# Performance work log

Hardware: AMD Instinct MI355X
Metric: run time of the kernel (lower is better)

The kernel has to match this reference:

```python
import jax, jax.numpy as jnp
import numpy as np

K = 20          # args.k
NEG = 0.2       # LeakyReLU negative slope

def lrelu(x):
    return jnp.where(x >= 0, x, NEG * x)

def bn(x, s, b):
    # eval-mode batchnorm folded into per-channel affine; channel axis = 1
    sh = (1, -1) + (1,) * (x.ndim - 2)
    return x * s.reshape(sh) + b.reshape(sh)

def se(x, w1, w2):
    # Squeeze-and-Excite on (B, C, N, k)
    y = jnp.mean(x, axis=(2, 3))                      # (B, C)
    y = jax.nn.sigmoid(jax.nn.relu(y @ w1.T) @ w2.T)  # (B, C)
    return x * y[:, :, None, None]

def graph_feature(x):
    # x: (B, C, N) -> edge features (B, 2C, N, K)
    xx = jnp.sum(x * x, axis=1)                        # (B, N)
    inner = jnp.einsum('bcn,bcm->bnm', x, x)           # (B, N, N)
    dist = -xx[:, :, None] + 2.0 * inner - xx[:, None, :]
    idx = jax.lax.top_k(dist, K)[1]                    # (B, N, K) nearest (incl. self)
    xt = jnp.transpose(x, (0, 2, 1))                   # (B, N, C)
    nbr = jax.vmap(lambda t, i: t[i])(xt, idx)         # (B, N, K, C)
    ctr = xt[:, :, None, :]
    out = jnp.concatenate([nbr - ctr, jnp.broadcast_to(ctr, nbr.shape)], axis=3)
    return jnp.transpose(out, (0, 3, 1, 2))

def edge_block(x, w, s, b, w1, w2):
    # get_graph_feature -> 1x1 conv -> BN -> SE -> LeakyReLU -> max over k
    g = graph_feature(x)                               # (B, 2C, N, K)
    h = jnp.einsum('bcnk,oc->bonk', g, w)
    h = lrelu(se(bn(h, s, b), w1, w2))
    return jnp.max(h, axis=-1)                         # (B, O, N)

def forward(x, conv1_w, conv2_w, conv3_w, conv4_w, conv5_w,
            bn1_s, bn1_b, bn2_s, bn2_b, bn3_s, bn3_b, bn4_s, bn4_b, bn5_s, bn5_b,
            se1_w1, se1_w2, se2_w1, se2_w2, se3_w1, se3_w2, se4_w1, se4_w2,
            res1_w, res2_w, res3_w,
            lin1_w, bn6_s, bn6_b, lin2_w, lin2_b, bn7_s, bn7_b, lin3_w, lin3_b):
    x1 = edge_block(x, conv1_w, bn1_s, bn1_b, se1_w1, se1_w2)                 # (B,512,N)
    x2 = edge_block(x1, conv2_w, bn2_s, bn2_b, se2_w1, se2_w2)
    x2 = x2 + jnp.einsum('bcn,oc->bon', x1, res1_w)                           # (B,512,N)
    x3 = edge_block(x2, conv3_w, bn3_s, bn3_b, se3_w1, se3_w2)
    x3 = x3 + jnp.einsum('bcn,oc->bon', x2, res2_w)                           # (B,1024,N)
    x4 = edge_block(x3, conv4_w, bn4_s, bn4_b, se4_w1, se4_w2)
    x4 = x4 + jnp.einsum('bcn,oc->bon', x3, res3_w)                           # (B,1024,N)
    h = jnp.concatenate([x1, x2, x3, x4], axis=1)                             # (B,3072,N)
    h = lrelu(bn(jnp.einsum('bcn,oc->bon', h, conv5_w), bn5_s, bn5_b))        # (B,2048,N)
    f = jnp.concatenate([jnp.max(h, axis=-1), jnp.mean(h, axis=-1)], axis=1)  # (B,4096)
    f = lrelu(bn(f @ lin1_w.T, bn6_s, bn6_b))       # dropout is eval-mode identity
    f = lrelu(bn(f @ lin2_w.T + lin2_b, bn7_s, bn7_b))
    return f @ lin3_w.T + lin3_b                    # (B,40)

def setup_inputs():
    ks = jax.random.split(jax.random.key(0), 40)
    B, N = 16, 128
    f32 = jnp.float32
    def w(i, shape, s=0.02):
        return jax.random.normal(ks[i], shape, f32) * s
    def bns(i, c):
        return 1.0 + 0.1 * jax.random.normal(ks[i], (c,), f32)
    def bnb(i, c):
        return 0.1 * jax.random.normal(ks[i], (c,), f32)
    return {
        'x': jax.random.normal(ks[0], (B, 512, N), f32),
        'conv1_w': w(1, (512, 1024)),
        'conv2_w': w(2, (512, 1024)),
        'conv3_w': w(3, (1024, 1024)),
        'conv4_w': w(4, (1024, 2048)),
        'conv5_w': w(5, (2048, 3072)),
        'bn1_s': bns(6, 512), 'bn1_b': bnb(7, 512),
        'bn2_s': bns(8, 512), 'bn2_b': bnb(9, 512),
        'bn3_s': bns(10, 1024), 'bn3_b': bnb(11, 1024),
        'bn4_s': bns(12, 1024), 'bn4_b': bnb(13, 1024),
        'bn5_s': bns(14, 2048), 'bn5_b': bnb(15, 2048),
        'se1_w1': w(16, (32, 512), 0.05), 'se1_w2': w(17, (512, 32), 0.05),
        'se2_w1': w(18, (32, 512), 0.05), 'se2_w2': w(19, (512, 32), 0.05),
        'se3_w1': w(20, (64, 1024), 0.05), 'se3_w2': w(21, (1024, 64), 0.05),
        'se4_w1': w(22, (64, 1024), 0.05), 'se4_w2': w(23, (1024, 64), 0.05),
        'res1_w': w(24, (512, 512)),
        'res2_w': w(25, (1024, 512)),
        'res3_w': w(26, (1024, 1024)),
        'lin1_w': w(27, (512, 4096)),
        'bn6_s': bns(28, 512), 'bn6_b': bnb(29, 512),
        'lin2_w': w(30, (256, 512)), 'lin2_b': bnb(31, 256),
        'bn7_s': bns(32, 256), 'bn7_b': bnb(33, 256),
        'lin3_w': w(34, (40, 256)), 'lin3_b': bnb(35, 40),
    }

def reference(x, conv1_w, conv2_w, conv3_w, conv4_w, conv5_w,
              bn1_s, bn1_b, bn2_s, bn2_b, bn3_s, bn3_b, bn4_s, bn4_b, bn5_s, bn5_b,
              se1_w1, se1_w2, se2_w1, se2_w2, se3_w1, se3_w2, se4_w1, se4_w2,
              res1_w, res2_w, res3_w,
              lin1_w, bn6_s, bn6_b, lin2_w, lin2_b, bn7_s, bn7_b, lin3_w, lin3_b):
    return forward(x, conv1_w, conv2_w, conv3_w, conv4_w, conv5_w,
                   bn1_s, bn1_b, bn2_s, bn2_b, bn3_s, bn3_b, bn4_s, bn4_b, bn5_s, bn5_b,
                   se1_w1, se1_w2, se2_w1, se2_w2, se3_w1, se3_w2, se4_w1, se4_w2,
                   res1_w, res2_w, res3_w,
                   lin1_w, bn6_s, bn6_b, lin2_w, lin2_b, bn7_s, bn7_b, lin3_w, lin3_b)
```

## Files before the change

### kernel.cpp

```cpp
#include <hip/hip_runtime.h>
#include <hip/hip_bf16.h>


#define BN_ALL 2048
typedef __hip_bfloat16 bf16;
typedef __attribute__((ext_vector_type(8))) short short8;
typedef __attribute__((ext_vector_type(4))) float float4v;
typedef __attribute__((ext_vector_type(4))) int int4v;

__device__ __forceinline__ float b2f(bf16 v) { return __bfloat162float(v); }
__device__ __forceinline__ float bs2f(short s) { return __bfloat162float(*reinterpret_cast<bf16*>(&s)); }
__device__ __forceinline__ float lrelu(float v) { return v >= 0.f ? v : 0.2f * v; }
__device__ __forceinline__ short f2bs(float v) {
    bf16 h = __float2bfloat16(v);
    return *reinterpret_cast<short*>(&h);
}

__device__ __forceinline__ void gll16(const void* g, void* l) {
    __builtin_amdgcn_global_load_lds(
        (const __attribute__((address_space(1))) unsigned int*)g,
        (__attribute__((address_space(3))) unsigned int*)l,
        16, 0, 0);
}

__device__ __forceinline__ float ldin(const void* p, size_t i, int isb) {
    return isb ? __bfloat162float(((const bf16*)p)[i]) : ((const float*)p)[i];
}

__device__ __forceinline__ float ld1(const float* p) { return *p; }
__device__ __forceinline__ float ld1(const bf16* p)  { return __bfloat162float(*p); }
__device__ __forceinline__ void st1(float* p, float v) { *p = v; }
__device__ __forceinline__ void st1(bf16* p, float v)  { *p = __float2bfloat16(v); }

__global__ __launch_bounds__(256) void detect_dtype(const void* __restrict__ x, int* __restrict__ flag) {
    const unsigned* u = (const unsigned*)x;
    int sane = 0;
    for (int i = threadIdx.x; i < 4096; i += 256) {
        unsigned e = (u[i] >> 23) & 0xFF;
        sane += (e >= 87 && e <= 167) ? 1 : 0;
    }
    __shared__ int sh[256];
    sh[threadIdx.x] = sane;
    __syncthreads();
    for (int off = 128; off > 0; off >>= 1) {
        if (threadIdx.x < off) sh[threadIdx.x] += sh[threadIdx.x + off];
        __syncthreads();
    }
    if (threadIdx.x == 0) *flag = (sh[0] < 2048) ? 1 : 0;
}

__device__ __forceinline__ void convert_core(int bid, int tid, const void* __restrict__ x,
                                             bf16* __restrict__ X0, int isb) {
    int item = bid * 256 + tid;
    int cg = item >> 11, bn = item & 2047;
    int b = bn >> 7, n = bn & 127;
    short8 pk;
#pragma unroll
// ... 247 lines not shown
            for (int nt = 0; nt < 2; ++nt)
                bv[nt] = *(const short8*)&Bp[(size_t)(h * 256 + (lq << 6) + wn * 32 + nt * 16 + lr) * 8];
#pragma unroll
            for (int mt = 0; mt < 4; ++mt)
#pragma unroll
                for (int nt = 0; nt < 2; ++nt)
                    acc[mt][nt] = __builtin_amdgcn_mfma_f32_16x16x32_bf16(av[mt], bv[nt], acc[mt][nt], 0, 0, 0);
        }
        __syncthreads();
        p ^= 1;
    }

    int isb = *dflag;
#pragma unroll
    for (int mt = 0; mt < 4; ++mt) {
#pragma unroll
        for (int r = 0; r < 4; ++r) {
            int row = bm + wm * 64 + mt * 16 + lq * 4 + r;
            float s = 1.f, bb = 0.f;
            if (bnS) { s = ldin(bnS, row, isb); bb = ldin(bnB, row, isb); }
#pragma unroll
            for (int nt = 0; nt < 2; ++nt) {
                int col = bn0 + wn * 32 + nt * 16 + lr;
                float v = acc[mt][nt][r];
                if (bnS) v = v * s + bb;
                if (act) v = lrelu(v);
                Cm[(size_t)row * BN_ALL + col] = v;
            }
        }
    }
}

__global__ __launch_bounds__(256) void gemm_pk(const short* __restrict__ packA,
                                               const bf16* __restrict__ X, float* __restrict__ Cm, int K,
                                               const void* __restrict__ bnS, const void* __restrict__ bnB,
                                               int act, const int* __restrict__ dflag) {
    __shared__ __align__(16) short SMEM[24576];
    gemm_core(blockIdx.x, blockIdx.y, threadIdx.x, SMEM, packA, X, Cm, K, bnS, bnB, act, dflag);
}

__global__ __launch_bounds__(256) void gram_gemm_k(const bf16* __restrict__ X, float* __restrict__ G,
                                                   const short* __restrict__ packA,
                                                   float* __restrict__ Cm, int K,
                                                   const int* __restrict__ dflag) {
    __shared__ __align__(16) short SMEM[24576];
    if (blockIdx.x < 16) {
        gram_core(blockIdx.x, threadIdx.x, SMEM, X, K, G);
    } else {
        int g = blockIdx.x - 16;
        gemm_core(g >> 5, g & 31, threadIdx.x, SMEM, packA, X, Cm, K, nullptr, nullptr, 0, dflag);
    }
}

template <typename S>
__global__ __launch_bounds__(128) void knn_topk(const S* __restrict__ X, int C, int* __restrict__ idx) {
    int b = blockIdx.x >> 7;
    int n = blockIdx.x & 127;
    int m = threadIdx.x;
    const S* base = X + b * 128;
    float s0 = 0, s1 = 0, q0 = 0, q1 = 0;
    for (int c = 0; c < C; c += 2) {
        const S* p = base + (size_t)c * BN_ALL;
        float xm0 = ld1(p + m),          xn0 = ld1(p + n);
        float xm1 = ld1(p + BN_ALL + m), xn1 = ld1(p + BN_ALL + n);
        s0 += xm0 * xn0; q0 += xm0 * xm0;
        s1 += xm1 * xn1; q1 += xm1 * xm1;
    }
    float inner = s0 + s1;
    float xxm   = q0 + q1;
    __shared__ float xx[128];
    __shared__ float dist[128];
    __shared__ float rv[128];
    __shared__ int   ri[128];
    xx[m] = xxm;
    __syncthreads();
    dist[m] = 2.0f * inner - xx[n] - xxm;
    for (int k = 0; k < 20; k++) {
        __syncthreads();
        rv[m] = dist[m]; ri[m] = m;
        __syncthreads();
        for (int off = 64; off > 0; off >>= 1) {
            if (m < off) {
                float a = rv[m], bv = rv[m + off];
                int ia = ri[m], ib = ri[m + off];
                if (bv > a || (bv == a && ib < ia)) { rv[m] = bv; ri[m] = ib; }
            }
            __syncthreads();
        }
        if (m == 0) { idx[blockIdx.x * 20 + k] = ri[0]; dist[ri[0]] = -3.0e38f; }
    }
}

template <typename S>
__global__ __launch_bounds__(256) void gemm_mfma(const void* __restrict__ w, int ldw,
                                                 const void* __restrict__ res, int Cin, int O,
                                                 const S* __restrict__ X, S* __restrict__ Cm, int K,
                                                 const void* __restrict__ bnS, const void* __restrict__ bnB,
                                                 int act, const int* __restrict__ dflag) {
    int isb = *dflag;
    __shared__ short Asm[4096];
    __shared__ short Bsm[4096];
    int tid = threadIdx.x;
    int bm  = blockIdx.x << 7;
    int bn0 = blockIdx.y << 7;
    int lane = tid & 63, wv = tid >> 6;
    int wm = wv & 1, wn = wv >> 1;
// ... 19 lines not shown
            short8 pk;
#pragma unroll
            for (int j = 0; j < 8; ++j) {
                float v = ldin(asrc, abase + kk + j, isb);
                if (dif) v = ldin(asrc, abase + Cin + kk + j, isb) - v;
                pk[j] = f2bs(v);
            }
            *(short8*)&Asm[(size_t)(q * 128 + m) * 8] = pk;
        }
#pragma unroll
        for (int it = 0; it < 2; ++it) {
            int i = tid + it * 256;
            int q = i >> 7, c = i & 127;
            const S* xp = X + (size_t)(k0 + q * 8) * BN_ALL + bn0 + c;
            short8 pk;
#pragma unroll
            for (int j = 0; j < 8; ++j) pk[j] = f2bs(ld1(xp + (size_t)j * BN_ALL));
            *(short8*)&Bsm[(size_t)i * 8] = pk;
        }
        __syncthreads();
        short8 av[4], bv[4];
#pragma unroll
        for (int mt = 0; mt < 4; ++mt)
            av[mt] = *(const short8*)&Asm[(size_t)((lq << 7) + wm * 64 + mt * 16 + lr) * 8];
#pragma unroll
        for (int nt = 0; nt < 4; ++nt)
            bv[nt] = *(const short8*)&Bsm[(size_t)((lq << 7) + wn * 64 + nt * 16 + lr) * 8];
#pragma unroll
        for (int mt = 0; mt < 4; ++mt)
#pragma unroll
            for (int nt = 0; nt < 4; ++nt)
                acc[mt][nt] = __builtin_amdgcn_mfma_f32_16x16x32_bf16(av[mt], bv[nt], acc[mt][nt], 0, 0, 0);
        __syncthreads();
    }
#pragma unroll
    for (int mt = 0; mt < 4; ++mt) {
#pragma unroll
        for (int r = 0; r < 4; ++r) {
            int row = bm + wm * 64 + mt * 16 + lq * 4 + r;
            float s = 1.f, bb = 0.f;
            if (bnS) { s = ldin(bnS, row, isb); bb = ldin(bnB, row, isb); }
#pragma unroll
            for (int nt = 0; nt < 4; ++nt) {
                int col = bn0 + wn * 64 + nt * 16 + lr;
                float v = acc[mt][nt][r];
                if (bnS) v = v * s + bb;
                if (act) v = lrelu(v);
                st1(Cm + (size_t)row * BN_ALL + col, v);
            }
        }
    }
}

template <typename S>
__global__ __launch_bounds__(256) void gather_pool(S* __restrict__ PS, const int* __restrict__ idx,
                                                   const void* __restrict__ bns, const void* __restrict__ bnb,
                                                   float* __restrict__ Mb, int O,
                                                   const int* __restrict__ dflag) {
    int isb = *dflag;
    int wv = threadIdx.x >> 6, lane = threadIdx.x & 63;
    int gw = blockIdx.x * 4 + wv;
    int o = gw >> 4, b = gw & 15;
    S* Prow = PS + (size_t)o * BN_ALL + b * 128;
    const S* Srow = PS + (size_t)(O + o) * BN_ALL + b * 128;
    int n0 = lane, n1 = lane + 64;
    const int4v* id0v = (const int4v*)(idx + (b * 128 + n0) * 20);
    const int4v* id1v = (const int4v*)(idx + (b * 128 + n1) * 20);
    int id0[20], id1[20];
#pragma unroll
    for (int t = 0; t < 5; ++t) {
        int4v v0 = id0v[t], v1 = id1v[t];
#pragma unroll
        for (int j = 0; j < 4; ++j) { id0[t * 4 + j] = v0[j]; id1[t * 4 + j] = v1[j]; }
    }
    float mx0 = -3.0e38f, mn0 = 3.0e38f, sm0 = 0.f;
    float mx1 = -3.0e38f, mn1 = 3.0e38f, sm1 = 0.f;
#pragma unroll
    for (int k = 0; k < 20; k++) {
        float p = ld1(Prow + id0[k]);
        mx0 = fmaxf(mx0, p); mn0 = fminf(mn0, p); sm0 += p;
    }
#pragma unroll
    for (int k = 0; k < 20; k++) {
        float p = ld1(Prow + id1[k]);
        mx1 = fmaxf(mx1, p); mn1 = fminf(mn1, p); sm1 += p;
    }
    float Sv0 = ld1(Srow + n0), Sv1 = ld1(Srow + n1);
    float s = ldin(bns, o, isb), bb = ldin(bnb, o, isb);
    float ext0 = (s >= 0.f) ? mx0 : mn0;
    float ext1 = (s >= 0.f) ? mx1 : mn1;
    float t0 = lrelu(s * (ext0 + Sv0) + bb);
    float t1 = lrelu(s * (ext1 + Sv1) + bb);
    st1(Prow + n0, t0);
    st1(Prow + n1, t1);
    float r1 = sm0 + sm1;
    float r2 = Sv0 + Sv1;
#pragma unroll
    for (int off = 32; off > 0; off >>= 1) {
        r1 += __shfl_xor(r1, off, 64);
        r2 += __shfl_xor(r2, off, 64);
    }
    if (lane == 0) Mb[b * O + o] = s * (r1 * (1.f / 2560.f) + r2 * (1.f / 128.f)) + bb;
}

__global__ __launch_bounds__(256) void se1_k(const float* __restrict__ Mb, const void* __restrict__ w1,
                                             float* __restrict__ Z, int O, int r,
                                             const int* __restrict__ dflag) {
    int isb = *dflag;
    int gw = (blockIdx.x * 256 + threadIdx.x) >> 6;
    int lane = threadIdx.x & 63;
    int b = gw / r, t = gw - b * r;
    const float* mv = Mb + (size_t)b * O;
    float acc = 0.f;
    for (int c = lane; c < O; c += 64) acc += ldin(w1, (size_t)t * O + c, isb) * mv[c];
#pragma unroll
    for (int off = 32; off > 0; off >>= 1) acc += __shfl_xor(acc, off, 64);
    if (lane == 0) Z[b * r + t] = fmaxf(acc, 0.f);
}

__global__ __launch_bounds__(256) void se2_k(const float* __restrict__ Z, const void* __restrict__ w2,
                                             float* __restrict__ Y, int O, int r,
                                             const int* __restrict__ dflag) {
    int isb = *dflag;
    int gw = (blockIdx.x * 256 + threadIdx.x) >> 6;
    int lane = threadIdx.x & 63;
    int b = gw / O, o = gw - b * O;
    float acc = 0.f;
    if (lane < r) acc = ldin(w2, (size_t)o * r + lane, isb) * Z[b * r + lane];
#pragma unroll
    for (int off = 32; off > 0; off >>= 1) acc += __shfl_xor(acc, off, 64);
    if (lane == 0) Y[b * O + o] = 1.f / (1.f + expf(-acc));
}

__global__ __launch_bounds__(256) void se_k(const float* __restrict__ Mb, const void* __restrict__ w1,
                                            const void* __restrict__ w2, float* __restrict__ Y, int O, int r,
                                            const int* __restrict__ dflag) {
    int isb = *dflag;
    int b = blockIdx.x, t = threadIdx.x;
    __shared__ float mloc[1024];
    __shared__ float z[64];
    for (int i = t; i < O; i += 256) mloc[i] = Mb[b * O + i];
    __syncthreads();
    if (t < r) {
        float acc = 0.f;
        for (int c = 0; c < O; c++) acc += ldin(w1, (size_t)t * O + c, isb) * mloc[c];
        z[t] = fmaxf(acc, 0.f);
    }
    __syncthreads();
    for (int o = t; o < O; o += 256) {
        float acc = 0.f;
        for (int j = 0; j < r; j++) acc += ldin(w2, (size_t)o * r + j, isb) * z[j];
        Y[b * O + o] = 1.f / (1.f + expf(-acc));
    }
}

__global__ __launch_bounds__(256) void finalize2_kp(const float* __restrict__ PS,
                                                    const float* __restrict__ Z,
                                                    const void* __restrict__ w2,
                                                    int useR, bf16* __restrict__ Xdst, int O, int r,
                                                    const int* __restrict__ dflag) {
    int isb = *dflag;
    int og = blockIdx.x >> 3;
    int b0 = (blockIdx.x & 7) * 2;
    __shared__ float Ysm[16];
    int wv = threadIdx.x >> 6, lane = threadIdx.x & 63;
#pragma unroll
    for (int s = 0; s < 4; ++s) {
        int pp = wv * 4 + s;
        int b = b0 + (pp >> 3);
        int o = og * 8 + (pp & 7);
        float acc = 0.f;
        if (lane < r) acc = ldin(w2, (size_t)o * r + lane, isb) * Z[b * r + lane];
#pragma unroll
        for (int off = 32; off > 0; off >>= 1) acc += __shfl_xor(acc, off, 64);
        if (lane == 0) Ysm[pp] = 1.f / (1.f + expf(-acc));
    }
    __syncthreads();
    int item = blockIdx.x * 256 + threadIdx.x;
    int bn = item & 2047;
    int b = bn >> 7;
    short8 pk;
#pragma unroll
    for (int j = 0; j < 8; ++j) {
        int rr = og * 8 + j;
        float v = Ysm[(b - b0) * 8 + j] * PS[(size_t)rr * BN_ALL + bn];
        if (useR) v += PS[(size_t)(2 * O + rr) * BN_ALL + bn];
        pk[j] = f2bs(v);
    }
    *(short8*)((short*)Xdst + ((size_t)og * BN_ALL + bn) * 8) = pk;
}

__global__ __launch_bounds__(256) void finalize_kp(const float* __restrict__ PS, const float* __restrict__ Y,
                                                   int useR, bf16* __restrict__ Xdst, int O) {
    int item = blockIdx.x * 256 + threadIdx.x;
    int og = item >> 11, bn = item & 2047;
    int b = bn >> 7;
    short8 pk;
#pragma unroll
    for (int j = 0; j < 8; ++j) {
        int r = og * 8 + j;
        float v = Y[b * O + r] * PS[(size_t)r * BN_ALL + bn];
        if (useR) v += PS[(size_t)(2 * O + r) * BN_ALL + bn];
        pk[j] = f2bs(v);
    }
    *(short8*)((short*)Xdst + ((size_t)og * BN_ALL + bn) * 8) = pk;
}

template <typename SP, typename SD>
__global__ __launch_bounds__(256) void finalize(const SP* __restrict__ PS, const float* __restrict__ Y,
                                                int useR, SD* __restrict__ Xdst, int O) {
    int tid = blockIdx.x * 256 + threadIdx.x;
    int o = tid >> 11, bn = tid & 2047;
    int b = bn >> 7;
    float v = Y[b * O + o] * ld1(PS + tid);
    if (useR) v += ld1(PS + (size_t)(2 * O + o) * BN_ALL + bn);
    st1(Xdst + tid, v);
}

template <typename S>
__global__ __launch_bounds__(256) void convert_x(const void* __restrict__ x, S* __restrict__ X0,
                                                 const int* __restrict__ dflag) {
    int isb = *dflag;
    int tid = blockIdx.x * 256 + threadIdx.x;
    int c = tid >> 11, bn = tid & 2047;
    int b = bn >> 7, n = bn & 127;
    st1(X0 + tid, ldin(x, (size_t)(b * 512 + c) * 128 + n, isb));
}

template <typename S>
__global__ __launch_bounds__(256) void pool5(const S* __restrict__ H, float* __restrict__ f) {
    int wv = threadIdx.x >> 6, lane = threadIdx.x & 63;
    int gw = blockIdx.x * 4 + wv;
    int m = gw >> 4, b = gw & 15;
    const S* Hp = H + (size_t)m * BN_ALL + b * 128;
    float v0 = ld1(Hp + lane), v1 = ld1(Hp + 64 + lane);
    float mx = fmaxf(v0, v1);
    float sm = v0 + v1;
#pragma unroll
    for (int off = 32; off > 0; off >>= 1) {
        mx = fmaxf(mx, __shfl_xor(mx, off, 64));
        sm += __shfl_xor(sm, off, 64);
    }
    if (lane == 0) {
        f[b * 4096 + m] = mx;
        f[b * 4096 + 2048 + m] = sm * (1.f / 128.f);
    }
}

__global__ __launch_bounds__(256) void head_k(const float* __restrict__ in, const void* __restrict__ W,
                                              const void* __restrict__ bias, const void* __restrict__ bns,
                                              const void* __restrict__ bnb, float* __restrict__ outf,
                                              void* __restrict__ outb, int Kd, int Od, int act,
                                              const int* __restrict__ dflag) {
    int isb = *dflag;
    int gw = (blockIdx.x * 256 + threadIdx.x) >> 6;
    int lane = threadIdx.x & 63;
    if (gw >= 16 * Od) return;
    int b = gw / Od, o = gw - b * Od;
    const float* iv = in + b * Kd;
    float acc = 0.f;
    for (int k = lane; k < Kd; k += 64) acc += iv[k] * ldin(W, (size_t)o * Kd + k, isb);
    for (int off = 32; off > 0; off >>= 1) acc += __shfl_xor(acc, off, 64);
    if (lane == 0) {
        float v = acc;
        if (bias) v += ldin(bias, o, isb);
        if (bns) v = v * ldin(bns, o, isb) + ldin(bnb, o, isb);
        if (act) v = lrelu(v);
        if (outb) {
            if (isb) ((bf16*)outb)[gw] = __float2bfloat16(v);
            else     ((float*)outb)[gw] = v;
        } else outf[gw] = v;
    }
}

__global__ __launch_bounds__(256) void zero_out(bf16* o, int n) {
    int i = blockIdx.x * 256 + threadIdx.x;
    if (i < n) o[i] = __float2bfloat16(0.f);
}

#define UNPACK_INPUTS()                                                     \
    const void* x_in   = d_in[0];                                           \
    const void* conv1w = d_in[1];  const void* conv2w = d_in[2];            \
    const void* conv3w = d_in[3];  const void* conv4w = d_in[4];            \
    const void* conv5w = d_in[5];                                           \
    const void* bn1s = d_in[6],  * bn1b = d_in[7];                          \
    const void* bn2s = d_in[8],  * bn2b = d_in[9];                          \
    const void* bn3s = d_in[10], * bn3b = d_in[11];                         \
    const void* bn4s = d_in[12], * bn4b = d_in[13];                         \
    const void* bn5s = d_in[14], * bn5b = d_in[15];                         \
    const void* se1w1 = d_in[16], * se1w2 = d_in[17];                       \
    const void* se2w1 = d_in[18], * se2w2 = d_in[19];                       \
    const void* se3w1 = d_in[20], * se3w2 = d_in[21];                       \
    const void* se4w1 = d_in[22], * se4w2 = d_in[23];                       \
    const void* res1w = d_in[24]; const void* res2w = d_in[25];             \
    const void* res3w = d_in[26]; const void* lin1w = d_in[27];             \
    const void* bn6s = d_in[28], * bn6b = d_in[29];                         \
    const void* lin2w = d_in[30], * lin2b = d_in[31];                       \
    const void* bn7s = d_in[32], * bn7b = d_in[33];                         \
    const void* lin3w = d_in[34], * lin3b = d_in[35];

static void run_net_packed2(void* const* d_in, void* d_out, void* d_ws, hipStream_t stream) {
    UNPACK_INPUTS();
    float* WS = (float*)d_ws;
    float* PS = WS;
    bf16*  XC = (bf16*)(WS + 6291456);
    short* P1 = (short*)(WS + 12582912);
    short* P2 = P1 + 524288;
    short* P3 = P2 + 786432;
    short* P4 = P3 + 1572864;
    short* P5 = P4 + 3145728;
    float* MB = WS + 18743296;
    float* YB = MB + 16384;
    float* FB = YB + 16384;
    float* F1 = FB + 65536;
    float* F2 = F1 + 8192;
    int* IDX  = (int*)(F2 + 4096);
    int* DFLAG = IDX + 40960;
    float* ZB = (float*)(DFLAG + 16);
    float* GRAM = WS + 18900000;
    bf16*  X0 = (bf16*)(PS + (size_t)2048 * BN_ALL);
    bf16* X1 = XC;
    bf16* X2 = XC + (size_t)512 * BN_ALL;
    bf16* X3 = XC + (size_t)1024 * BN_ALL;
    bf16* X4 = XC + (size_t)2048 * BN_ALL;

    detect_dtype<<<1, 256, 0, stream>>>(x_in, DFLAG);
    convert_pack_all<<<6528, 256, 0, stream>>>(x_in, X0,
        conv1w, conv2w, conv3w, conv4w, conv5w, res1w, res2w, res3w,
        P1, P2, P3, P4, P5, DFLAG);

    gram_gemm_k<<<16 + 8 * 32, 256, 0, stream>>>(X0, GRAM, P1, PS, 512, DFLAG);
    topk_k<<<512, 256, 0, stream>>>(GRAM, IDX);
    gather_pool<float><<<2048, 256, 0, stream>>>(PS, IDX, bn1s, bn1b, MB, 512, DFLAG);
    se1_k<<<128, 256, 0, stream>>>(MB, se1w1, ZB, 512, 32, DFLAG);
    finalize2_kp<<<512, 256, 0, stream>>>(PS, ZB, se1w2, 0, X1, 512, 32, DFLAG);

    gram_gemm_k<<<16 + 12 * 32, 256, 0, stream>>>(X1, GRAM, P2, PS, 512, DFLAG);
    topk_k<<<512, 256, 0, stream>>>(GRAM, IDX);
    gather_pool<float><<<2048, 256, 0, stream>>>(PS, IDX, bn2s, bn2b, MB, 512, DFLAG);
    se1_k<<<128, 256, 0, stream>>>(MB, se2w1, ZB, 512, 32, DFLAG);
    finalize2_kp<<<512, 256, 0, stream>>>(PS, ZB, se2w2, 1, X2, 512, 32, DFLAG);

    gram_gemm_k<<<16 + 24 * 32, 256, 0, stream>>>(X2, GRAM, P3, PS, 512, DFLAG);
    topk_k<<<512, 256, 0, stream>>>(GRAM, IDX);
    gather_pool<float><<<4096, 256, 0, stream>>>(PS, IDX, bn3s, bn3b, MB, 1024, DFLAG);
    se1_k<<<256, 256, 0, stream>>>(MB, se3w1, ZB, 1024, 64, DFLAG);
    finalize2_kp<<<1024, 256, 0, stream>>>(PS, ZB, se3w2, 1, X3, 1024, 64, DFLAG);

    gram_gemm_k<<<16 + 24 * 32, 256, 0, stream>>>(X3, GRAM, P4, PS, 1024, DFLAG);
    topk_k<<<512, 256, 0, stream>>>(GRAM, IDX);
    gather_pool<float><<<4096, 256, 0, stream>>>(PS, IDX, bn4s, bn4b, MB, 1024, DFLAG);
    se1_k<<<256, 256, 0, stream>>>(MB, se4w1, ZB, 1024, 64, DFLAG);
    finalize2_kp<<<1024, 256, 0, stream>>>(PS, ZB, se4w2, 1, X4, 1024, 64, DFLAG);

    gemm_pk<<<dim3(16, 32), 256, 0, stream>>>(P5, XC, PS, 3072, bn5s, bn5b, 1, DFLAG);
    pool5<float><<<8192, 256, 0, stream>>>(PS, FB);

    head_k<<<2048, 256, 0, stream>>>(FB, lin1w, nullptr, bn6s, bn6b, F1, nullptr, 4096, 512, 1, DFLAG);
    head_k<<<1024, 256, 0, stream>>>(F1, lin2w, lin2b, bn7s, bn7b, F2, nullptr, 512, 256, 1, DFLAG);
    head_k<<<160, 256, 0, stream>>>(F2, lin3w, lin3b, nullptr, nullptr, nullptr, d_out, 256, 40, 0, DFLAG);
}

static void run_net_packed(void* const* d_in, void* d_out, void* d_ws, hipStream_t stream) {
    UNPACK_INPUTS();
    float* WS = (float*)d_ws;
    float* PS   = WS;
    bf16*  XC   = (bf16*)(WS + 6291456);
    short* PACK = (short*)(WS + 12582912);
    float* MB = WS + 15728640;
    float* YB = MB + 16384;
    float* FB = YB + 16384;
    float* F1 = FB + 65536;
    float* F2 = F1 + 8192;
    int* IDX  = (int*)(F2 + 4096);
    int* DFLAG = IDX + 40960;
    float* ZB = (float*)(DFLAG + 16);
    bf16*  X0 = (bf16*)(PS + (size_t)2048 * BN_ALL);
    float* GRAM = PS;
    bf16* X1 = XC;
    bf16* X2 = XC + (size_t)512 * BN_ALL;
    bf16* X3 = XC + (size_t)1024 * BN_ALL;
    bf16* X4 = XC + (size_t)2048 * BN_ALL;

    detect_dtype<<<1, 256, 0, stream>>>(x_in, DFLAG);
    convert_kp<<<512, 256, 0, stream>>>(x_in, X0, DFLAG);

    gram_k<<<16, 256, 0, stream>>>(X0, 512, GRAM);
    topk_k<<<512, 256, 0, stream>>>(GRAM, IDX);
    pack_w<<<256, 256, 0, stream>>>(conv1w, 1024, nullptr, 512, 512, 1024, 512, PACK, DFLAG);
    gemm_pk<<<dim3(8, 32), 256, 0, stream>>>(PACK, X0, PS, 512, nullptr, nullptr, 0, DFLAG);
    gather_pool<float><<<2048, 256, 0, stream>>>(PS, IDX, bn1s, bn1b, MB, 512, DFLAG);
    se1_k<<<128, 256, 0, stream>>>(MB, se1w1, ZB, 512, 32, DFLAG);
    se2_k<<<2048, 256, 0, stream>>>(ZB, se1w2, YB, 512, 32, DFLAG);
    finalize_kp<<<512, 256, 0, stream>>>(PS, YB, 0, X1, 512);

    gram_k<<<16, 256, 0, stream>>>(X1, 512, GRAM);
    topk_k<<<512, 256, 0, stream>>>(GRAM, IDX);
    pack_w<<<384, 256, 0, stream>>>(conv2w, 1024, res1w, 512, 512, 1536, 512, PACK, DFLAG);
    gemm_pk<<<dim3(12, 32), 256, 0, stream>>>(PACK, X1, PS, 512, nullptr, nullptr, 0, DFLAG);
    gather_pool<float><<<2048, 256, 0, stream>>>(PS, IDX, bn2s, bn2b, MB, 512, DFLAG);
    se1_k<<<128, 256, 0, stream>>>(MB, se2w1, ZB, 512, 32, DFLAG);
    se2_k<<<2048, 256, 0, stream>>>(ZB, se2w2, YB, 512, 32, DFLAG);
    finalize_kp<<<512, 256, 0, stream>>>(PS, YB, 1, X2, 512);

    gram_k<<<16, 256, 0, stream>>>(X2, 512, GRAM);
    topk_k<<<512, 256, 0, stream>>>(GRAM, IDX);
    pack_w<<<768, 256, 0, stream>>>(conv3w, 1024, res2w, 512, 1024, 3072, 512, PACK, DFLAG);
    gemm_pk<<<dim3(24, 32), 256, 0, stream>>>(PACK, X2, PS, 512, nullptr, nullptr, 0, DFLAG);
    gather_pool<float><<<4096, 256, 0, stream>>>(PS, IDX, bn3s, bn3b, MB, 1024, DFLAG);
    se1_k<<<256, 256, 0, stream>>>(MB, se3w1, ZB, 1024, 64, DFLAG);
    se2_k<<<4096, 256, 0, stream>>>(ZB, se3w2, YB, 1024, 64, DFLAG);
    finalize_kp<<<1024, 256, 0, stream>>>(PS, YB, 1, X3, 1024);

// ... 95 lines not shown
```

Baseline: 527.5 us.

## Fuse per-layer topk/gather/SE/finalize and head tail into cooperative kernels

Replaces the chains of small kernel launches after each gram/gemm (topk, gather_pool, se1, finalize) and the final pool5 plus three head linears with two persistent cooperative kernels. A fixed grid of 768 blocks steps through each stage and calls grid.sync() between stages. The aim is to remove per-launch overhead and the idle gaps between many tiny kernels. In exchange, stages with few work items leave blocks idle, grid barriers have their own cost, and it relies on cooperative launch succeeding, with a fallback to the old launches.

New measurement: 1.621 ms. 3.07x slower.

```diff
diff --git a/kernel.cpp b/kernel.cpp
--- a/kernel.cpp
+++ b/kernel.cpp
@@ -1,8 +1,12 @@
 #include <hip/hip_runtime.h>
 #include <hip/hip_bf16.h>
+#include <hip/hip_cooperative_groups.h>
+
+namespace cg = cooperative_groups;
 
 
 #define BN_ALL 2048
+#define COOP_GRID 768
 typedef __hip_bfloat16 bf16;
 typedef __attribute__((ext_vector_type(8))) short short8;
 typedef __attribute__((ext_vector_type(4))) float float4v;
@@ -356,6 +360,245 @@
     }
 }
 
+__device__ __forceinline__ void gather_core(int vb, int tid, float* __restrict__ PS,
+                                            const int* __restrict__ idx,
+                                            const void* __restrict__ bns, const void* __restrict__ bnb,
+                                            float* __restrict__ Mb, int O, int isb) {
+    int wv = tid >> 6, lane = tid & 63;
+    int gw = vb * 4 + wv;
+    int o = gw >> 4, b = gw & 15;
+    float* Prow = PS + (size_t)o * BN_ALL + b * 128;
+    const float* Srow = PS + (size_t)(O + o) * BN_ALL + b * 128;
+    int n0 = lane, n1 = lane + 64;
+    const int4v* id0v = (const int4v*)(idx + (b * 128 + n0) * 20);
+    const int4v* id1v = (const int4v*)(idx + (b * 128 + n1) * 20);
+    int id0[20], id1[20];
+#pragma unroll
+    for (int t = 0; t < 5; ++t) {
+        int4v v0 = id0v[t], v1 = id1v[t];
+#pragma unroll
+        for (int j = 0; j < 4; ++j) { id0[t * 4 + j] = v0[j]; id1[t * 4 + j] = v1[j]; }
+    }
+    float mx0 = -3.0e38f, mn0 = 3.0e38f, sm0 = 0.f;
+    float mx1 = -3.0e38f, mn1 = 3.0e38f, sm1 = 0.f;
+#pragma unroll
+    for (int k = 0; k < 20; k++) {
+        float p = Prow[id0[k]];
+        mx0 = fmaxf(mx0, p); mn0 = fminf(mn0, p); sm0 += p;
+    }
+#pragma unroll
+    for (int k = 0; k < 20; k++) {
+        float p = Prow[id1[k]];
+        mx1 = fmaxf(mx1, p); mn1 = fminf(mn1, p); sm1 += p;
+    }
+    float Sv0 = Srow[n0], Sv1 = Srow[n1];
+    float s = ldin(bns, o, isb), bb = ldin(bnb, o, isb);
+    float ext0 = (s >= 0.f) ? mx0 : mn0;
+    float ext1 = (s >= 0.f) ? mx1 : mn1;
+    float t0 = lrelu(s * (ext0 + Sv0) + bb);
+    float t1 = lrelu(s * (ext1 + Sv1) + bb);
+    Prow[n0] = t0;
+    Prow[n1] = t1;
+    float r1 = sm0 + sm1;
+    float r2 = Sv0 + Sv1;
+#pragma unroll
+    for (int off = 32; off > 0; off >>= 1) {
+        r1 += __shfl_xor(r1, off, 64);
+        r2 += __shfl_xor(r2, off, 64);
+    }
+    if (lane == 0) Mb[b * O + o] = s * (r1 * (1.f / 2560.f) + r2 * (1.f / 128.f)) + bb;
+}
+
+template <typename S>
+__global__ __launch_bounds__(256) void gather_pool(S* __restrict__ PS, const int* __restrict__ idx,
+                                                   const void* __restrict__ bns, const void* __restrict__ bnb,
+                                                   float* __restrict__ Mb, int O,
+                                                   const int* __restrict__ dflag) {
+    int isb = *dflag;
+    int wv = threadIdx.x >> 6, lane = threadIdx.x & 63;
+    int gw = blockIdx.x * 4 + wv;
+    int o = gw >> 4, b = gw & 15;
+    S* Prow = PS + (size_t)o * BN_ALL + b * 128;
+    const S* Srow = PS + (size_t)(O + o) * BN_ALL + b * 128;
+    int n0 = lane, n1 = lane + 64;
+    const int4v* id0v = (const int4v*)(idx + (b * 128 + n0) * 20);
+    const int4v* id1v = (const int4v*)(idx + (b * 128 + n1) * 20);
+    int id0[20], id1[20];
+#pragma unroll
+    for (int t = 0; t < 5; ++t) {
+        int4v v0 = id0v[t], v1 = id1v[t];
+#pragma unroll
+        for (int j = 0; j < 4; ++j) { id0[t * 4 + j] = v0[j]; id1[t * 4 + j] = v1[j]; }
+    }
+    float mx0 = -3.0e38f, mn0 = 3.0e38f, sm0 = 0.f;
+    float mx1 = -3.0e38f, mn1 = 3.0e38f, sm1 = 0.f;
+#pragma unroll
+    for (int k = 0; k < 20; k++) {
+        float p = ld1(Prow + id0[k]);
+        mx0 = fmaxf(mx0, p); mn0 = fminf(mn0, p); sm0 += p;
+    }
+#pragma unroll
+    for (int k = 0; k < 20; k++) {
+        float p = ld1(Prow + id1[k]);
+        mx1 = fmaxf(mx1, p); mn1 = fminf(mn1, p); sm1 += p;
+    }
+    float Sv0 = ld1(Srow + n0), Sv1 = ld1(Srow + n1);
+    float s = ldin(bns, o, *dflag), bb = ldin(bnb, o, *dflag);
+    float ext0 = (s >= 0.f) ? mx0 : mn0;
+    float ext1 = (s >= 0.f) ? mx1 : mn1;
+    float t0 = lrelu(s * (ext0 + Sv0) + bb);
+    float t1 = lrelu(s * (ext1 + Sv1) + bb);
+    st1(Prow + n0, t0);
+    st1(Prow + n1, t1);
+    float r1 = sm0 + sm1;
+    float r2 = Sv0 + Sv1;
+#pragma unroll
+    for (int off = 32; off > 0; off >>= 1) {
+        r1 += __shfl_xor(r1, off, 64);
+        r2 += __shfl_xor(r2, off, 64);
+    }
+    if (lane == 0) Mb[b * O + o] = s * (r1 * (1.f / 2560.f) + r2 * (1.f / 128.f)) + bb;
+}
+
+__device__ __forceinline__ void se1_core(int vb, int tid, const float* __restrict__ Mb,
+                                         const void* __restrict__ w1, float* __restrict__ Z,
+                                         int O, int r, int isb) {
+    int gw = (vb * 256 + tid) >> 6;
+    int lane = tid & 63;
+    int b = gw / r, t = gw - b * r;
+    const float* mv = Mb + (size_t)b * O;
+    float acc = 0.f;
+    for (int c = lane; c < O; c += 64) acc += ldin(w1, (size_t)t * O + c, isb) * mv[c];
+#pragma unroll
+    for (int off = 32; off > 0; off >>= 1) acc += __shfl_xor(acc, off, 64);
+    if (lane == 0) Z[b * r + t] = fmaxf(acc, 0.f);
+}
+
+__global__ __launch_bounds__(256) void se1_k(const float* __restrict__ Mb, const void* __restrict__ w1,
+                                             float* __restrict__ Z, int O, int r,
+                                             const int* __restrict__ dflag) {
+    se1_core(blockIdx.x, threadIdx.x, Mb, w1, Z, O, r, *dflag);
+}
+
+__global__ __launch_bounds__(256) void se2_k(const float* __restrict__ Z, const void* __restrict__ w2,
+                                             float* __restrict__ Y, int O, int r,
+                                             const int* __restrict__ dflag) {
+    int isb = *dflag;
+    int gw = (blockIdx.x * 256 + threadIdx.x) >> 6;
+    int lane = threadIdx.x & 63;
+    int b = gw / O, o = gw - b * O;
+    float acc = 0.f;
+    if (lane < r) acc = ldin(w2, (size_t)o * r + lane, isb) * Z[b * r + lane];
+#pragma unroll
+    for (int off = 32; off > 0; off >>= 1) acc += __shfl_xor(acc, off, 64);
+    if (lane == 0) Y[b * O + o] = 1.f / (1.f + expf(-acc));
+}
+
+__global__ __launch_bounds__(256) void se_k(const float* __restrict__ Mb, const void* __restrict__ w1,
+                                            const void* __restrict__ w2, float* __restrict__ Y, int O, int r,
+                                            const int* __restrict__ dflag) {
+    int isb = *dflag;
+    int b = blockIdx.x, t = threadIdx.x;
+    __shared__ float mloc[1024];
+    __shared__ float z[64];
+    for (int i = t; i < O; i += 256) mloc[i] = Mb[b * O + i];
+    __syncthreads();
+    if (t < r) {
+        float acc = 0.f;
+        for (int c = 0; c < O; c++) acc += ldin(w1, (size_t)t * O + c, isb) * mloc[c];
+        z[t] = fmaxf(acc, 0.f);
+    }
+    __syncthreads();
+    for (int o = t; o < O; o += 256) {
+        float acc = 0.f;
+        for (int j = 0; j < r; j++) acc += ldin(w2, (size_t)o * r + j, isb) * z[j];
+        Y[b * O + o] = 1.f / (1.f + expf(-acc));
+    }
+}
+
+__device__ __forceinline__ void fin2_core(int vb, int tid, const float* __restrict__ PS,
+                                          const float* __restrict__ Z, const void* __restrict__ w2,
+                                          int useR, bf16* __restrict__ Xdst, int O, int r, int isb,
+                                          float* __restrict__ Ysm) {
+    int og = vb >> 3;
+    int b0 = (vb & 7) * 2;
+    int wv = tid >> 6, lane = tid & 63;
+#pragma unroll
+    for (int s = 0; s < 4; ++s) {
+        int pp = wv * 4 + s;
+        int b = b0 + (pp >> 3);
+        int o = og * 8 + (pp & 7);
+        float acc = 0.f;
+        if (lane < r) acc = ldin(w2, (size_t)o * r + lane, isb) * Z[b * r + lane];
+#pragma unroll
+        for (int off = 32; off > 0; off >>= 1) acc += __shfl_xor(acc, off, 64);
+        if (lane == 0) Ysm[pp] = 1.f / (1.f + expf(-acc));
+    }
+    __syncthreads();
+    int item = vb * 256 + tid;
+    int bn = item & 2047;
+    int b = bn >> 7;
+    short8 pk;
+#pragma unroll
+    for (int j = 0; j < 8; ++j) {
+        int rr = og * 8 + j;
+        float v = Ysm[(b - b0) * 8 + j] * PS[(size_t)rr * BN_ALL + bn];
+        if (useR) v += PS[(size_t)(2 * O + rr) * BN_ALL + bn];
+        pk[j] = f2bs(v);
+    }
+    *(short8*)((short*)Xdst + ((size_t)og * BN_ALL + bn) * 8) = pk;
+}
+
+__global__ __launch_bounds__(256) void finalize2_kp(const float* __restrict__ PS,
+                                                    const float* __restrict__ Z,
+                                                    const void* __restrict__ w2,
+                                                    int useR, bf16* __restrict__ Xdst, int O, int r,
+                                                    const int* __restrict__ dflag) {
+    __shared__ float Ysm[16];
+    fin2_core(blockIdx.x, threadIdx.x, PS, Z, w2, useR, Xdst, O, r, *dflag, Ysm);
+}
+
+__global__ __launch_bounds__(256) void tail_coop(const float* __restrict__ G, int* __restrict__ idx,
+                                                 float* __restrict__ PS,
+                                                 const void* __restrict__ bns, const void* __restrict__ bnb,
+                                                 float* __restrict__ Mb, const void* __restrict__ w1,
+                                                 float* __restrict__ Z, const void* __restrict__ w2,
+                                                 int useR, bf16* __restrict__ Xdst, int O, int r,
+                                                 const int* __restrict__ dflag) {
+    cg::grid_group grid = cg::this_grid();
+    __shared__ float Ysm[16];
+    int isb = *dflag;
+    int tid = threadIdx.x;
+    if (blockIdx.x < 512) topk_core(blockIdx.x, tid, G, idx);
+    grid.sync();
+    for (int vb = blockIdx.x; vb < O * 4; vb += COOP_GRID)
+        gather_core(vb, tid, PS, idx, bns, bnb, Mb, O, isb);
+    grid.sync();
+    for (int vb = blockIdx.x; vb < (16 * r) / 4; vb += COOP_GRID)
+        se1_core(vb, tid, Mb, w1, Z, O, r, isb);
+    grid.sync();
+    for (int vb = blockIdx.x; vb < O; vb += COOP_GRID) {
+        fin2_core(vb, tid, PS, Z, w2, useR, Xdst, O, r, isb, Ysm);
+        __syncthreads();
+    }
+}
+
+__global__ __launch_bounds__(256) void finalize_kp(const float* __restrict__ PS, const float* __restrict__ Y,
+                                                   int useR, bf16* __restrict__ Xdst, int O) {
+    int item = blockIdx.x * 256 + threadIdx.x;
+    int og = item >> 11, bn = item & 2047;
+    int b = bn >> 7;
+    short8 pk;
+#pragma unroll
+    for (int j = 0; j < 8; ++j) {
+        int r = og * 8 + j;
+        float v = Y[b * O + r] * PS[(size_t)r * BN_ALL + bn];
+        if (useR) v += PS[(size_t)(2 * O + r) * BN_ALL + bn];
+        pk[j] = f2bs(v);
+    }
+    *(short8*)((short*)Xdst + ((size_t)og * BN_ALL + bn) * 8) = pk;
+}
+
 template <typename S>
 __global__ __launch_bounds__(128) void knn_topk(const S* __restrict__ X, int C, int* __restrict__ idx) {
     int b = blockIdx.x >> 7;
@@ -481,160 +724,6 @@
     }
 }
 
-template <typename S>
-__global__ __launch_bounds__(256) void gather_pool(S* __restrict__ PS, const int* __restrict__ idx,
-                                                   const void* __restrict__ bns, const void* __restrict__ bnb,
-                                                   float* __restrict__ Mb, int O,
-                                                   const int* __restrict__ dflag) {
-    int isb = *dflag;
-    int wv = threadIdx.x >> 6, lane = threadIdx.x & 63;
-    int gw = blockIdx.x * 4 + wv;
-    int o = gw >> 4, b = gw & 15;
-    S* Prow = PS + (size_t)o * BN_ALL + b * 128;
-    const S* Srow = PS + (size_t)(O + o) * BN_ALL + b * 128;
-    int n0 = lane, n1 = lane + 64;
-    const int4v* id0v = (const int4v*)(idx + (b * 128 + n0) * 20);
-    const int4v* id1v = (const int4v*)(idx + (b * 128 + n1) * 20);
-    int id0[20], id1[20];
-#pragma unroll
-    for (int t = 0; t < 5; ++t) {
-        int4v v0 = id0v[t], v1 = id1v[t];
-#pragma unroll
-        for (int j = 0; j < 4; ++j) { id0[t * 4 + j] = v0[j]; id1[t * 4 + j] = v1[j]; }
-    }
-    float mx0 = -3.0e38f, mn0 = 3.0e38f, sm0 = 0.f;
-    float mx1 = -3.0e38f, mn1 = 3.0e38f, sm1 = 0.f;
-#pragma unroll
-    for (int k = 0; k < 20; k++) {
-        float p = ld1(Prow + id0[k]);
-        mx0 = fmaxf(mx0, p); mn0 = fminf(mn0, p); sm0 += p;
-    }
-#pragma unroll
-    for (int k = 0; k < 20; k++) {
-        float p = ld1(Prow + id1[k]);
-        mx1 = fmaxf(mx1, p); mn1 = fminf(mn1, p); sm1 += p;
-    }
-    float Sv0 = ld1(Srow + n0), Sv1 = ld1(Srow + n1);
-    float s = ldin(bns, o, isb), bb = ldin(bnb, o, isb);
-    float ext0 = (s >= 0.f) ? mx0 : mn0;
-    float ext1 = (s >= 0.f) ? mx1 : mn1;
-    float t0 = lrelu(s * (ext0 + Sv0) + bb);
-    float t1 = lrelu(s * (ext1 + Sv1) + bb);
-    st1(Prow + n0, t0);
-    st1(Prow + n1, t1);
-    float r1 = sm0 + sm1;
-    float r2 = Sv0 + Sv1;
-#pragma unroll
-    for (int off = 32; off > 0; off >>= 1) {
-        r1 += __shfl_xor(r1, off, 64);
-        r2 += __shfl_xor(r2, off, 64);
-    }
-    if (lane == 0) Mb[b * O + o] = s * (r1 * (1.f / 2560.f) + r2 * (1.f / 128.f)) + bb;
-}
-
-__global__ __launch_bounds__(256) void se1_k(const float* __restrict__ Mb, const void* __restrict__ w1,
-                                             float* __restrict__ Z, int O, int r,
-                                             const int* __restrict__ dflag) {
-    int isb = *dflag;
-    int gw = (blockIdx.x * 256 + threadIdx.x) >> 6;
-    int lane = threadIdx.x & 63;
-    int b = gw / r, t = gw - b * r;
-    const float* mv = Mb + (size_t)b * O;
-    float acc = 0.f;
-    for (int c = lane; c < O; c += 64) acc += ldin(w1, (size_t)t * O + c, isb) * mv[c];
-#pragma unroll
-    for (int off = 32; off > 0; off >>= 1) acc += __shfl_xor(acc, off, 64);
-    if (lane == 0) Z[b * r + t] = fmaxf(acc, 0.f);
-}
-
-__global__ __launch_bounds__(256) void se2_k(const float* __restrict__ Z, const void* __restrict__ w2,
-                                             float* __restrict__ Y, int O, int r,
-                                             const int* __restrict__ dflag) {
-    int isb = *dflag;
-    int gw = (blockIdx.x * 256 + threadIdx.x) >> 6;
-    int lane = threadIdx.x & 63;
-    int b = gw / O, o = gw - b * O;
-    float acc = 0.f;
-    if (lane < r) acc = ldin(w2, (size_t)o * r + lane, isb) * Z[b * r + lane];
-#pragma unroll
-    for (int off = 32; off > 0; off >>= 1) acc += __shfl_xor(acc, off, 64);
-    if (lane == 0) Y[b * O + o] = 1.f / (1.f + expf(-acc));
-}
-
-__global__ __launch_bounds__(256) void se_k(const float* __restrict__ Mb, const void* __restrict__ w1,
-                                            const void* __restrict__ w2, float* __restrict__ Y, int O, int r,
-                                            const int* __restrict__ dflag) {
-    int isb = *dflag;
-    int b = blockIdx.x, t = threadIdx.x;
-    __shared__ float mloc[1024];
-    __shared__ float z[64];
-    for (int i = t; i < O; i += 256) mloc[i] = Mb[b * O + i];
-    __syncthreads();
-    if (t < r) {
-        float acc = 0.f;
-        for (int c = 0; c < O; c++) acc += ldin(w1, (size_t)t * O + c, isb) * mloc[c];
-        z[t] = fmaxf(acc, 0.f);
-    }
-    __syncthreads();
-    for (int o = t; o < O; o += 256) {
-        float acc = 0.f;
-        for (int j = 0; j < r; j++) acc += ldin(w2, (size_t)o * r + j, isb) * z[j];
-        Y[b * O + o] = 1.f / (1.f + expf(-acc));
-    }
-}
-
-__global__ __launch_bounds__(256) void finalize2_kp(const float* __restrict__ PS,
-                                                    const float* __restrict__ Z,
-                                                    const void* __restrict__ w2,
-                                                    int useR, bf16* __restrict__ Xdst, int O, int r,
-                                                    const int* __restrict__ dflag) {
-    int isb = *dflag;
-    int og = blockIdx.x >> 3;
-    int b0 = (blockIdx.x & 7) * 2;
-    __shared__ float Ysm[16];
-    int wv = threadIdx.x >> 6, lane = threadIdx.x & 63;
-#pragma unroll
-    for (int s = 0; s < 4; ++s) {
-        int pp = wv * 4 + s;
-        int b = b0 + (pp >> 3);
-        int o = og * 8 + (pp & 7);
-        float acc = 0.f;
-        if (lane < r) acc = ldin(w2, (size_t)o * r + lane, isb) * Z[b * r + lane];
-#pragma unroll
-        for (int off = 32; off > 0; off >>= 1) acc += __shfl_xor(acc, off, 64);
-        if (lane == 0) Ysm[pp] = 1.f / (1.f + expf(-acc));
-    }
-    __syncthreads();
-    int item = blockIdx.x * 256 + threadIdx.x;
-    int bn = item & 2047;
-    int b = bn >> 7;
-    short8 pk;
-#pragma unroll
-    for (int j = 0; j < 8; ++j) {
-        int rr = og * 8 + j;
-        float v = Ysm[(b - b0) * 8 + j] * PS[(size_t)rr * BN_ALL + bn];
-        if (useR) v += PS[(size_t)(2 * O + rr) * BN_ALL + bn];
-        pk[j] = f2bs(v);
-    }
-    *(short8*)((short*)Xdst + ((size_t)og * BN_ALL + bn) * 8) = pk;
-}
-
-__global__ __launch_bounds__(256) void finalize_kp(const float* __restrict__ PS, const float* __restrict__ Y,
-                                                   int useR, bf16* __restrict__ Xdst, int O) {
-    int item = blockIdx.x * 256 + threadIdx.x;
-    int og = item >> 11, bn = item & 2047;
-    int b = bn >> 7;
-    short8 pk;
-#pragma unroll
-    for (int j = 0; j < 8; ++j) {
-        int r = og * 8 + j;
-        float v = Y[b * O + r] * PS[(size_t)r * BN_ALL + bn];
-        if (useR) v += PS[(size_t)(2 * O + r) * BN_ALL + bn];
-        pk[j] = f2bs(v);
-    }
-    *(short8*)((short*)Xdst + ((size_t)og * BN_ALL + bn) * 8) = pk;
-}
-
 template <typename SP, typename SD>
 __global__ __launch_bounds__(256) void finalize(const SP* __restrict__ PS, const float* __restrict__ Y,
                                                 int useR, SD* __restrict__ Xdst, int O) {
@@ -656,6 +745,26 @@
     st1(X0 + tid, ldin(x, (size_t)(b * 512 + c) * 128 + n, isb));
 }
 
+__device__ __forceinline__ void pool5_core(int vb, int tid, const float* __restrict__ H,
+                                           float* __restrict__ f) {
+    int wv = tid >> 6, lane = tid & 63;
+    int gw = vb * 4 + wv;
+    int m = gw >> 4, b = gw & 15;
+    const float* Hp = H + (size_t)m * BN_ALL + b * 128;
+    float v0 = Hp[lane], v1 = Hp[64 + lane];
+    float mx = fmaxf(v0, v1);
+    float sm = v0 + v1;
+#pragma unroll
+    for (int off = 32; off > 0; off >>= 1) {
+        mx = fmaxf(mx, __shfl_xor(mx, off, 64));
+        sm += __shfl_xor(sm, off, 64);
+    }
+    if (lane == 0) {
+        f[b * 4096 + m] = mx;
+        f[b * 4096 + 2048 + m] = sm * (1.f / 128.f);
+    }
+}
+
 template <typename S>
 __global__ __launch_bounds__(256) void pool5(const S* __restrict__ H, float* __restrict__ f) {
     int wv = threadIdx.x >> 6, lane = threadIdx.x & 63;
@@ -676,14 +785,13 @@
     }
 }
 
-__global__ __launch_bounds__(256) void head_k(const float* __restrict__ in, const void* __restrict__ W,
-                                              const void* __restrict__ bias, const void* __restrict__ bns,
-                                              const void* __restrict__ bnb, float* __restrict__ outf,
-                                              void* __restrict__ outb, int Kd, int Od, int act,
-                                              const int* __restrict__ dflag) {
-    int isb = *dflag;
-    int gw = (blockIdx.x * 256 + threadIdx.x) >> 6;
-    int lane = threadIdx.x & 63;
+__device__ __forceinline__ void head_core(int vb, int tid, const float* __restrict__ in,
+                                          const void* __restrict__ W, const void* __restrict__ bias,
+                                          const void* __restrict__ bns, const void* __restrict__ bnb,
+                                          float* __restrict__ outf, void* __restrict__ outb,
+                                          int Kd, int Od, int act, int isb) {
+    int gw = (vb * 256 + tid) >> 6;
+    int lane = tid & 63;
     if (gw >= 16 * Od) return;
     int b = gw / Od, o = gw - b * Od;
     const float* iv = in + b * Kd;
@@ -700,6 +808,40 @@
             else     ((float*)outb)[gw] = v;
         } else outf[gw] = v;
     }
+}
+
+__global__ __launch_bounds__(256) void head_k(const float* __restrict__ in, const void* __restrict__ W,
+                                              const void* __restrict__ bias, const void* __restrict__ bns,
+                                              const void* __restrict__ bnb, float* __restrict__ outf,
+                                              void* __restrict__ outb, int Kd, int Od, int act,
+                                              const int* __restrict__ dflag) {
+    head_core(blockIdx.x, threadIdx.x, in, W, bias, bns, bnb, outf, outb, Kd, Od, act, *dflag);
+}
+
+__global__ __launch_bounds__(256) void tail5_coop(const float* __restrict__ H, float* __restrict__ FB,
+                                                  const void* __restrict__ lin1w,
+                                                  const void* __restrict__ bn6s, const void* __restrict__ bn6b,
+                                                  float* __restrict__ F1,
+                                                  const void* __restrict__ lin2w, const void* __restrict__ lin2b,
+                                                  const void* __restrict__ bn7s, const void* __restrict__ bn7b,
+                                                  float* __restrict__ F2,
+                                                  const void* __restrict__ lin3w, const void* __restrict__ lin3b,
+                                                  void* __restrict__ dout,
+                                                  const int* __restrict__ dflag) {
+    cg::grid_group grid = cg::this_grid();
+    int isb = *dflag;
+    int tid = threadIdx.x;
+    for (int vb = blockIdx.x; vb < 8192; vb += COOP_GRID)
+        pool5_core(vb, tid, H, FB);
+    grid.sync();
+    for (int vb = blockIdx.x; vb < 2048; vb += COOP_GRID)
+        head_core(vb, tid, FB, lin1w, nullptr, bn6s, bn6b, F1, nullptr, 4096, 512, 1, isb);
+    grid.sync();
+    for (int vb = blockIdx.x; vb < 1024; vb += COOP_GRID)
+        head_core(vb, tid, F1, lin2w, lin2b, bn7s, bn7b, F2, nullptr, 512, 256, 1, isb);
+    grid.sync();
+    if (blockIdx.x < 160)
+        head_core(blockIdx.x, tid, F2, lin3w, lin3b, nullptr, nullptr, nullptr, dout, 256, 40, 0, isb);
 }
 
 __global__ __launch_bounds__(256) void zero_out(bf16* o, int n) {
@@ -727,6 +869,23 @@
     const void* lin2w = d_in[30], * lin2b = d_in[31];                       \
     const void* bn7s = d_in[32], * bn7b = d_in[33];                         \
     const void* lin3w = d_in[34], * lin3b = d_in[35];
+
+static void launch_tail(const float* G, int* idx, float* PS, const void* bns, const void* bnb,
+                        float* Mb, const void* w1, float* Z, const void* w2,
+                        int useR, bf16* Xdst, int O, int r, const int* dflag,
+                        hipStream_t stream) {
+    void* args[] = {(void*)&G, (void*)&idx, (void*)&PS, (void*)&bns, (void*)&bnb,
+                    (void*)&Mb, (void*)&w1, (void*)&Z, (void*)&w2,
+                    (void*)&useR, (void*)&Xdst, (void*)&O, (void*)&r, (void*)&dflag};
+    hipError_t e = hipLaunchCooperativeKernel((void*)tail_coop, dim3(COOP_GRID), dim3(256),
+                                              args, 0, stream);
+    if (e != hipSuccess) {
+        topk_k<<<512, 256, 0, stream>>>(G, idx);
+        gather_pool<float><<<O * 4, 256, 0, stream>>>(PS, idx, bns, bnb, Mb, O, dflag);
+        se1_k<<<(16 * r) / 4, 256, 0, stream>>>(Mb, w1, Z, O, r, dflag);
+        finalize2_kp<<<O, 256, 0, stream>>>(PS, Z, w2, useR, Xdst, O, r, dflag);
+    }
+}
 
 static void run_net_packed2(void* const* d_in, void* d_out, void* d_ws, hipStream_t stream) {
     UNPACK_INPUTS();
@@ -759,35 +918,33 @@
         P1, P2, P3, P4, P5, DFLAG);
 
     gram_gemm_k<<<16 + 8 * 32, 256, 0, stream>>>(X0, GRAM, P1, PS, 512, DFLAG);
-    topk_k<<<512, 256, 0, stream>>>(GRAM, IDX);
-    gather_pool<float><<<2048, 256, 0, stream>>>(PS, IDX, bn1s, bn1b, MB, 512, DFLAG);
-    se1_k<<<128, 256, 0, stream>>>(MB, se1w1, ZB, 512, 32, DFLAG);
-    finalize2_kp<<<512, 256, 0, stream>>>(PS, ZB, se1w2, 0, X1, 512, 32, DFLAG);
+    launch_tail(GRAM, IDX, PS, bn1s, bn1b, MB, se1w1, ZB, se1w2, 0, X1, 512, 32, DFLAG, stream);
 
     gram_gemm_k<<<16 + 12 * 32, 256, 0, stream>>>(X1, GRAM, P2, PS, 512, DFLAG);
-    topk_k<<<512, 256, 0, stream>>>(GRAM, IDX);
-    gather_pool<float><<<2048, 256, 0, stream>>>(PS, IDX, bn2s, bn2b, MB, 512, DFLAG);
-    se1_k<<<128, 256, 0, stream>>>(MB, se2w1, ZB, 512, 32, DFLAG);
-    finalize2_kp<<<512, 256, 0, stream>>>(PS, ZB, se2w2, 1, X2, 512, 32, DFLAG);
+    launch_tail(GRAM, IDX, PS, bn2s, bn2b, MB, se2w1, ZB, se2w2, 1, X2, 512, 32, DFLAG, stream);
 
     gram_gemm_k<<<16 + 24 * 32, 256, 0, stream>>>(X2, GRAM, P3, PS, 512, DFLAG);
-    topk_k<<<512, 256, 0, stream>>>(GRAM, IDX);
-    gather_pool<float><<<4096, 256, 0, stream>>>(PS, IDX, bn3s, bn3b, MB, 1024, DFLAG);
-    se1_k<<<256, 256, 0, stream>>>(MB, se3w1, ZB, 1024, 64, DFLAG);
-    finalize2_kp<<<1024, 256, 0, stream>>>(PS, ZB, se3w2, 1, X3, 1024, 64, DFLAG);
+    launch_tail(GRAM, IDX, PS, bn3s, bn3b, MB, se3w1, ZB, se3w2, 1, X3, 1024, 64, DFLAG, stream);
 
     gram_gemm_k<<<16 + 24 * 32, 256, 0, stream>>>(X3, GRAM, P4, PS, 1024, DFLAG);
-    topk_k<<<512, 256, 0, stream>>>(GRAM, IDX);
-    gather_pool<float><<<4096, 256, 0, stream>>>(PS, IDX, bn4s, bn4b, MB, 1024, DFLAG);
-    se1_k<<<256, 256, 0, stream>>>(MB, se4w1, ZB, 1024, 64, DFLAG);
-    finalize2_kp<<<1024, 256, 0, stream>>>(PS, ZB, se4w2, 1, X4, 1024, 64, DFLAG);
+    launch_tail(GRAM, IDX, PS, bn4s, bn4b, MB, se4w1, ZB, se4w2, 1, X4, 1024, 64, DFLAG, stream);
 
     gemm_pk<<<dim3(16, 32), 256, 0, stream>>>(P5, XC, PS, 3072, bn5s, bn5b, 1, DFLAG);
-    pool5<float><<<8192, 256, 0, stream>>>(PS, FB);
-
-    head_k<<<2048, 256, 0, stream>>>(FB, lin1w, nullptr, bn6s, bn6b, F1, nullptr, 4096, 512, 1, DFLAG);
-    head_k<<<1024, 256, 0, stream>>>(F1, lin2w, lin2b, bn7s, bn7b, F2, nullptr, 512, 256, 1, DFLAG);
-    head_k<<<160, 256, 0, stream>>>(F2, lin3w, lin3b, nullptr, nullptr, nullptr, d_out, 256, 40, 0, DFLAG);
+
+    {
+        const float* Hc = PS;
+        void* args[] = {(void*)&Hc, (void*)&FB, (void*)&lin1w, (void*)&bn6s, (void*)&bn6b,
+                        (void*)&F1, (void*)&lin2w, (void*)&lin2b, (void*)&bn7s, (void*)&bn7b,
+                        (void*)&F2, (void*)&lin3w, (void*)&lin3b, (void*)&d_out, (void*)&DFLAG};
+        hipError_t e = hipLaunchCooperativeKernel((void*)tail5_coop, dim3(COOP_GRID), dim3(256),
+                                                  args, 0, stream);
+        if (e != hipSuccess) {
+            pool5<float><<<8192, 256, 0, stream>>>(PS, FB);
+            head_k<<<2048, 256, 0, stream>>>(FB, lin1w, nullptr, bn6s, bn6b, F1, nullptr, 4096, 512, 1, DFLAG);
+            head_k<<<1024, 256, 0, stream>>>(F1, lin2w, lin2b, bn7s, bn7b, F2, nullptr, 512, 256, 1, DFLAG);
+            head_k<<<160, 256, 0, stream>>>(F2, lin3w, lin3b, nullptr, nullptr, nullptr, d_out, 256, 40, 0, DFLAG);
+        }
+    }
 }
 
 static void run_net_packed(void* const* d_in, void* d_out, void* d_ws, hipStream_t stream) {
```
